# Optimization experiments

Measured on AMD Instinct MI355X. Metric: run time of the kernel, lower is better.

## Reference

```python
import jax, jax.numpy as jnp
import numpy as np

D_MODEL = 1024
EXPAND = 2
D_INNER = EXPAND * D_MODEL      # 2048
D_STATE = 2
D_CONV = 4
DT_RANK = (D_MODEL + 15) // 16  # 64
BATCH, SEQ = 2, 4096
LN_EPS = 1e-5


def setup_inputs() -> dict:
    key = jax.random.key(0)
    ks = jax.random.split(key, 16)
    s = 0.02
    inp = {
        "x":       jax.random.normal(ks[0], (BATCH, SEQ, D_MODEL), jnp.float32),
        # Mamba params (torch Linear convention: W is [out, in])
        "w_in":    jax.random.normal(ks[1], (2 * D_INNER, D_MODEL), jnp.float32) * s,
        "conv_w":  jax.random.normal(ks[2], (D_INNER, 1, D_CONV), jnp.float32) * s,
        "conv_b":  jnp.zeros((D_INNER,), jnp.float32),
        "w_xproj": jax.random.normal(ks[3], (DT_RANK + 2 * D_STATE, D_INNER), jnp.float32) * s,
        "w_dt":    jax.random.normal(ks[4], (D_INNER, DT_RANK), jnp.float32) * s,
        "b_dt":    jax.random.normal(ks[5], (D_INNER,), jnp.float32) * s - 4.0,  # softplus -> small dt
        "a_log":   jnp.log(jnp.broadcast_to(jnp.arange(1, D_STATE + 1, dtype=jnp.float32), (D_INNER, D_STATE))),
        "d_skip":  jnp.ones((D_INNER,), jnp.float32),
        "w_out":   jax.random.normal(ks[6], (D_MODEL, D_INNER), jnp.float32) * s,
        # LayerNorms
        "ln1_g":   jnp.ones((D_MODEL,), jnp.float32),
        "ln1_b":   jnp.zeros((D_MODEL,), jnp.float32),
        "ln2_g":   jnp.ones((D_MODEL,), jnp.float32),
        "ln2_b":   jnp.zeros((D_MODEL,), jnp.float32),
        # FFN (Linear d->d, ReLU, Linear d->d; dropout inactive at eval)
        "ffn_w1":  jax.random.normal(ks[7], (D_MODEL, D_MODEL), jnp.float32) * s,
        "ffn_b1":  jnp.zeros((D_MODEL,), jnp.float32),
        "ffn_w2":  jax.random.normal(ks[8], (D_MODEL, D_MODEL), jnp.float32) * s,
        "ffn_b2":  jnp.zeros((D_MODEL,), jnp.float32),
    }
    return inp


def _ln(x, g, b):
    mu = x.mean(-1, keepdims=True)
    v = ((x - mu) ** 2).mean(-1, keepdims=True)
    return (x - mu) * jax.lax.rsqrt(v + LN_EPS) * g + b


def _mamba(x, w_in, conv_w, conv_b, w_xproj, w_dt, b_dt, a_log, d_skip, w_out):
    Bsz = x.shape[0]
    xz = x @ w_in.T                      # (B,L,2*D_INNER)
    xp, z = jnp.split(xz, 2, axis=-1)
    # depthwise causal conv over time
    xc = jnp.transpose(xp, (0, 2, 1))    # (B,D,L)
    xc = jax.lax.conv_general_dilated(
        xc, conv_w, window_strides=(1,), padding=[(D_CONV - 1, 0)],
        feature_group_count=D_INNER)
    xc = xc + conv_b[None, :, None]
    xp = jax.nn.silu(jnp.transpose(xc, (0, 2, 1)))   # (B,L,D)
    # input-dependent SSM params
    x_dbl = xp @ w_xproj.T               # (B,L,DT_RANK+2N)
    dt, Bm, Cm = jnp.split(x_dbl, [DT_RANK, DT_RANK + D_STATE], axis=-1)
    dt = jax.nn.softplus(dt @ w_dt.T + b_dt)          # (B,L,D)
    A = -jnp.exp(a_log)                  # (D,N)
    dA = jnp.exp(dt[..., None] * A)                  # (B,L,D,N)
    dBu = dt[..., None] * Bm[:, :, None, :] * xp[..., None]  # (B,L,D,N)

    def step(h, inp):
        da, dbu, c = inp                 # (B,D,N),(B,D,N),(B,N)
        h = da * h + dbu
        y = jnp.einsum('bdn,bn->bd', h, c)
        return h, y

    h0 = jnp.zeros((Bsz, D_INNER, D_STATE), x.dtype)
    _, ys = jax.lax.scan(step, h0, (jnp.swapaxes(dA, 0, 1),
                                    jnp.swapaxes(dBu, 0, 1),
                                    jnp.swapaxes(Cm, 0, 1)))
    y = jnp.swapaxes(ys, 0, 1)           # (B,L,D)
    y = (y + d_skip * xp) * jax.nn.silu(z)
    return y @ w_out.T                   # (B,L,d_model)


def reference(x, w_in, conv_w, conv_b, w_xproj, w_dt, b_dt, a_log, d_skip, w_out,
              ln1_g, ln1_b, ln2_g, ln2_b, ffn_w1, ffn_b1, ffn_w2, ffn_b2):
    h = x + _mamba(_ln(x, ln1_g, ln1_b), w_in, conv_w, conv_b, w_xproj,
                   w_dt, b_dt, a_log, d_skip, w_out)
    f = _ln(h, ln2_g, ln2_b)
    f = jax.nn.relu(f @ ffn_w1.T + ffn_b1) @ ffn_w2.T + ffn_b2
    return h + f
```

## Files before the change

kernel.cpp:

```cpp
#include <hip/hip_runtime.h>

typedef unsigned short u16;
typedef __bf16 bf16x8 __attribute__((ext_vector_type(8)));
typedef float f32x4 __attribute__((ext_vector_type(4)));
typedef float f32x2 __attribute__((ext_vector_type(2)));
typedef u16 u16x4 __attribute__((ext_vector_type(4)));
typedef u16 u16x8 __attribute__((ext_vector_type(8)));

#define SEQ   4096
#define DM    1024
#define DI    2048
#define NTOK  8192
#define NXP   68
#define DTR   64
#define NCH   4096
#define CHUNK 32
#define NCHK  128

__device__ __forceinline__ float bf2f(u16 v) {
  union { unsigned u; float f; } x; x.u = ((unsigned)v) << 16; return x.f;
}
__device__ __forceinline__ u16 f2bf(float f) {
  unsigned u = __float_as_uint(f);
  return (u16)((u + 0x7FFFu + ((u >> 16) & 1u)) >> 16);
}

__device__ __forceinline__ void g2l16(const u16* g, u16* l) {
  __builtin_amdgcn_global_load_lds(
      (const __attribute__((address_space(1))) unsigned int*)g,
      (__attribute__((address_space(3))) unsigned int*)l, 16, 0, 0);
}

__global__ __launch_bounds__(256)
void detect_kernel(const u16* __restrict__ x, int* __restrict__ flag)
{
  __shared__ int tot;
  if (threadIdx.x == 0) tot = 0;
  __syncthreads();
  int cnt = 0;
  for (int i = threadIdx.x; i < 4096; i += 256) {
    const int e = (x[2 * i] >> 7) & 0xFF;
    if (e > 167) cnt++;
  }
  atomicAdd(&tot, cnt);
  __syncthreads();
  if (threadIdx.x == 0) flag[0] = (tot >= 8) ? 1 : 0;
}

#define NW0 4194304
#define NW1  139264
#define NW2  131072
#define NW3 2097152
#define NW4 1048576
#define NW5 1048576
#define NBB 4228
__global__ __launch_bounds__(256)
void convert_all(const float* __restrict__ s0, const float* __restrict__ s1,
                 const float* __restrict__ s2, const float* __restrict__ s3,
                 const float* __restrict__ s4, const float* __restrict__ s5,
                 u16* __restrict__ d0, u16* __restrict__ d1, u16* __restrict__ d2,
                 u16* __restrict__ d3, u16* __restrict__ d4, u16* __restrict__ d5,
                 const void* t0, const void* t1, const void* t2, const void* t3,
                 const void* t4, const void* t5, const void* t6, const void* t7,
                 const void* t8, const void* t9, const void* t10,
                 u16* __restrict__ dsm, const int* __restrict__ flag)
{
  if (blockIdx.x >= NBB) {
    const int i = (blockIdx.x - NBB) * 256 + threadIdx.x;
    if (i >= 24576) return;
    const void* src; int off; int dsti = i;
    if      (i < 8192)  { src = t0;  off = i;
                          dsti = (off & 3) * DI + (off >> 2); }
    else if (i < 10240) { src = t1;  off = i - 8192; }
    else if (i < 12288) { src = t2;  off = i - 10240; }
    else if (i < 16384) { src = t3;  off = i - 12288; }
    else if (i < 18432) { src = t4;  off = i - 16384; }
    else if (i < 19456) { src = t5;  off = i - 18432; }
    else if (i < 20480) { src = t6;  off = i - 19456; }
    else if (i < 21504) { src = t7;  off = i - 20480; }
    else if (i < 22528) { src = t8;  off = i - 21504; }
    else if (i < 23552) { src = t9;  off = i - 22528; }
    else                { src = t10; off = i - 23552; }
    dsm[dsti] = (*flag) ? f2bf(((const float*)src)[off]) : ((const u16*)src)[off];
    return;
  }
  if (*flag == 0) return;
  long e = ((long)blockIdx.x * 256 + threadIdx.x) * 8;
  const long c1 = NW0, c2 = c1 + NW1, c3 = c2 + NW2, c4 = c3 + NW3,
             c5 = c4 + NW4, c6 = c5 + NW5;
  if (e >= c6) return;
  const float* s; u16* d;
  if      (e < c1) { s = s0;          d = d0; }
  else if (e < c2) { s = s1; e -= c1; d = d1; }
  else if (e < c3) { s = s2; e -= c2; d = d2; }
  else if (e < c4) { s = s3; e -= c3; d = d3; }
  else if (e < c5) { s = s4; e -= c4; d = d4; }
  else             { s = s5; e -= c5; d = d5; }
  f32x4 a = *(const f32x4*)(s + e);
  f32x4 b = *(const f32x4*)(s + e + 4);
  u16x8 o;
#pragma unroll
  for (int k = 0; k < 4; ++k) { o[k] = f2bf(a[k]); o[4 + k] = f2bf(b[k]); }
  *(u16x8*)(d + e) = o;
}

template<bool DUAL>
__global__ __launch_bounds__(256)
void ln_kernel(const void* __restrict__ xin, const u16* __restrict__ gw,
               const u16* __restrict__ bw, u16* __restrict__ outp,
               const int* __restrict__ flag)
{
  const int tid = threadIdx.x;
  const int sub = tid >> 7;
  const int col0 = (tid & 127) * 8;
  const int row = blockIdx.x * 2 + sub;
  const bool isf32 = DUAL ? (*flag != 0) : true;
  float v[8];
  if (isf32) {
    const float* xf = (const float*)xin + (size_t)row * DM + col0;
    f32x4 a = *(const f32x4*)xf, b2 = *(const f32x4*)(xf + 4);
#pragma unroll
    for (int k = 0; k < 4; ++k) { v[k] = a[k]; v[4 + k] = b2[k]; }
  } else {
    u16x8 xb = *(const u16x8*)((const u16*)xin + (size_t)row * DM + col0);
#pragma unroll
    for (int k = 0; k < 8; ++k) v[k] = bf2f(xb[k]);
  }
  float s = 0.f, s2 = 0.f;
#pragma unroll
  for (int k = 0; k < 8; ++k) { s += v[k]; s2 += v[k] * v[k]; }
#pragma unroll
  for (int off = 32; off > 0; off >>= 1) {
    s  += __shfl_down(s,  off);
    s2 += __shfl_down(s2, off);
  }
  __shared__ float red[4], red2[4];
  __shared__ f32x2 stat[2];
  const int wv = tid >> 6;
  if ((tid & 63) == 0) { red[wv] = s; red2[wv] = s2; }
  __syncthreads();
  if ((tid & 127) == 0) {
    float ts = red[sub * 2] + red[sub * 2 + 1];
    float t2 = red2[sub * 2] + red2[sub * 2 + 1];
    float mu = ts * (1.f / DM);
    float var = t2 * (1.f / DM) - mu * mu;
    stat[sub] = f32x2{mu, rsqrtf(var + 1e-5f)};
  }
  __syncthreads();
  const float mu = stat[sub][0], rs = stat[sub][1];
  u16x8 gv = *(const u16x8*)(gw + col0), bv = *(const u16x8*)(bw + col0);
  u16x8 o;
#pragma unroll
  for (int k = 0; k < 8; ++k)
    o[k] = f2bf((v[k] - mu) * rs * bf2f(gv[k]) + bf2f(bv[k]));
  *(u16x8*)(outp + (size_t)row * DM + col0) = o;
}

template<int EPI, int LNBX>
__global__ __launch_bounds__(256, 2)
void gemm_kernel(const u16* __restrict__ A, const u16* __restrict__ Bc,
                 const u16* __restrict__ Braw,
                 int M, int N, int K,
                 const u16* __restrict__ bias, const u16* __restrict__ addbf,
                 const float* __restrict__ addf, const int* __restrict__ dtflag,
                 void* __restrict__ Cp, void* __restrict__ Cp2)
{
  __shared__ __align__(16) u16 sA[2][128 * 32];
  __shared__ __align__(16) u16 sB[2][128 * 32];
  const int fl = *dtflag;
  const u16* __restrict__ B = fl ? Bc : Braw;
  const int tid = threadIdx.x;
  const int b = blockIdx.x;
  const int xcd = b & 7;
  const int kk = b >> 3;
  const int bx = kk & ((1 << LNBX) - 1);
  const int by = xcd * 8 + (kk >> LNBX);
  const int m0 = by * 128;
  const int n0 = bx * 128;
  const int lane = tid & 63;
  const int wv = tid >> 6;
  const int wm = (wv & 1) * 64;
  const int wn = (wv >> 1) * 64;
  const int r = lane & 15;
  const int q = lane >> 4;
  const int rsw = (r >> 1) & 3;

  const int pr = lane >> 2;
  const int kc = (lane & 3) ^ ((pr >> 1) & 3);
  const int pk = kc * 8;
  u16* lA0[2] = { &sA[0][(wv * 2 + 0) * 512], &sA[1][(wv * 2 + 0) * 512] };
  u16* lA1[2] = { &sA[0][(wv * 2 + 1) * 512], &sA[1][(wv * 2 + 1) * 512] };
  u16* lB0[2] = { &sB[0][(wv * 2 + 0) * 512], &sB[1][(wv * 2 + 0) * 512] };
  u16* lB1[2] = { &sB[0][(wv * 2 + 1) * 512], &sB[1][(wv * 2 + 1) * 512] };
  const u16* gA0 = A + (size_t)(m0 + wv * 32 + pr) * K + pk;
  const u16* gA1 = gA0 + (size_t)16 * K;
  const u16* gB0 = B + (size_t)(n0 + wv * 32 + pr) * K + pk;
  const u16* gB1 = gB0 + (size_t)16 * K;

  f32x4 acc[4][4];
#pragma unroll
  for (int i = 0; i < 4; ++i)
#pragma unroll
    for (int j = 0; j < 4; ++j)
#pragma unroll
      for (int t = 0; t < 4; ++t) acc[i][j][t] = 0.f;

  g2l16(gA0, lA0[0]); g2l16(gA1, lA1[0]);
  g2l16(gB0, lB0[0]); g2l16(gB1, lB1[0]);

  const int nk = K >> 5;
  for (int kt = 0; kt < nk; ++kt) {
    const int cur = kt & 1;
    __syncthreads();
    bf16x8 af[4], bfr[4];
#pragma unroll
    for (int i = 0; i < 4; ++i)
      af[i] = *reinterpret_cast<const bf16x8*>(
          &sA[cur][(wm + i * 16 + r) * 32 + (q ^ rsw) * 8]);
#pragma unroll
    for (int j = 0; j < 4; ++j)
      bfr[j] = *reinterpret_cast<const bf16x8*>(
          &sB[cur][(wn + j * 16 + r) * 32 + (q ^ rsw) * 8]);
    if (kt + 1 < nk) {
      gA0 += 32; gA1 += 32; gB0 += 32; gB1 += 32;
      g2l16(gA0, lA0[cur ^ 1]); g2l16(gA1, lA1[cur ^ 1]);
      g2l16(gB0, lB0[cur ^ 1]); g2l16(gB1, lB1[cur ^ 1]);
    }
#pragma unroll
    for (int i = 0; i < 4; ++i)
#pragma unroll
      for (int j = 0; j < 4; ++j)
        acc[i][j] = __builtin_amdgcn_mfma_f32_16x16x32_bf16(af[i], bfr[j], acc[i][j], 0, 0, 0);
  }

#pragma unroll
  for (int i = 0; i < 4; ++i) {
#pragma unroll
    for (int j = 0; j < 4; ++j) {
#pragma unroll
      for (int t = 0; t < 4; ++t) {
        const int row = m0 + wm + i * 16 + q * 4 + t;
        const int col = n0 + wn + j * 16 + r;
        float v = acc[i][j][t];
        if (EPI == 6) {
          const size_t rb = (size_t)row * DI;
          if (col < DI) ((u16*)Cp)[rb + col] = f2bf(v);
          else          ((u16*)Cp2)[rb + col - DI] = f2bf(v);
        } else {
          const size_t idx = (size_t)row * N + col;
          if (EPI == 1) {
            ((u16*)Cp)[idx] = f2bf(v);
          } else if (EPI == 2) {
            v += bf2f(bias[col]);
            v = (v > 15.f) ? v : __logf(1.f + __expf(v));
            ((u16*)Cp)[idx] = f2bf(v);
          } else if (EPI == 3) {
            v += fl ? addf[idx] : bf2f(addbf[idx]);
            ((float*)Cp)[idx] = v;
          } else if (EPI == 4) {
            v += bf2f(bias[col]);
            ((u16*)Cp)[idx] = f2bf(fmaxf(v, 0.f));
          } else {
            v += bf2f(bias[col]) + addf[idx];
            if (fl) ((float*)Cp)[idx] = v;
            else    ((u16*)Cp)[idx] = f2bf(v);
          }
        }
      }
    }
  }
}

__global__ __launch_bounds__(256, 2)
void xproj_splitk(const u16* __restrict__ A, const u16* __restrict__ Bc,
                  const u16* __restrict__ Braw, const int* __restrict__ dtflag,
                  float* __restrict__ part)
{
  __shared__ __align__(16) u16 sA[2][128 * 32];
  __shared__ __align__(16) u16 sB[2][128 * 32];
  const int fl = *dtflag;
  const u16* __restrict__ B = fl ? Bc : Braw;
  const int tid = threadIdx.x;
  const int kz = blockIdx.x;
  const int m0 = blockIdx.y * 128;
  const int kbase = kz * 256;
  const int lane = tid & 63;
  const int wv = tid >> 6;
  const int wm = (wv & 1) * 64;
  const int wn = (wv >> 1) * 64;
  const int r = lane & 15;
  const int q = lane >> 4;
  const int rsw = (r >> 1) & 3;
  const int pr = lane >> 2;
  const int kc = (lane & 3) ^ ((pr >> 1) & 3);
  const int pk = kc * 8;

  u16* lA0[2] = { &sA[0][(wv * 2 + 0) * 512], &sA[1][(wv * 2 + 0) * 512] };
  u16* lA1[2] = { &sA[0][(wv * 2 + 1) * 512], &sA[1][(wv * 2 + 1) * 512] };
  u16* lB0[2] = { &sB[0][(wv * 2 + 0) * 512], &sB[1][(wv * 2 + 0) * 512] };
  u16* lB1[2] = { &sB[0][(wv * 2 + 1) * 512], &sB[1][(wv * 2 + 1) * 512] };
  int br0 = wv * 32 + pr;      if (br0 > 67) br0 = 67;
  int br1 = wv * 32 + 16 + pr; if (br1 > 67) br1 = 67;
  const u16* gA0 = A + (size_t)(m0 + wv * 32 + pr) * DI + kbase + pk;
  const u16* gA1 = gA0 + (size_t)16 * DI;
  const u16* gB0 = B + (size_t)br0 * DI + kbase + pk;
  const u16* gB1 = B + (size_t)br1 * DI + kbase + pk;

  f32x4 acc[4][4];
#pragma unroll
  for (int i = 0; i < 4; ++i)
#pragma unroll
    for (int j = 0; j < 4; ++j)
#pragma unroll
      for (int t = 0; t < 4; ++t) acc[i][j][t] = 0.f;

  g2l16(gA0, lA0[0]); g2l16(gA1, lA1[0]);
  g2l16(gB0, lB0[0]); g2l16(gB1, lB1[0]);

  for (int kt = 0; kt < 8; ++kt) {
    const int cur = kt & 1;
    __syncthreads();
    bf16x8 af[4], bfr[4];
#pragma unroll
    for (int i = 0; i < 4; ++i)
      af[i] = *reinterpret_cast<const bf16x8*>(
          &sA[cur][(wm + i * 16 + r) * 32 + (q ^ rsw) * 8]);
#pragma unroll
    for (int j = 0; j < 4; ++j)
      bfr[j] = *reinterpret_cast<const bf16x8*>(
          &sB[cur][(wn + j * 16 + r) * 32 + (q ^ rsw) * 8]);
    if (kt + 1 < 8) {
      gA0 += 32; gA1 += 32; gB0 += 32; gB1 += 32;
      g2l16(gA0, lA0[cur ^ 1]); g2l16(gA1, lA1[cur ^ 1]);
      g2l16(gB0, lB0[cur ^ 1]); g2l16(gB1, lB1[cur ^ 1]);
    }
#pragma unroll
    for (int i = 0; i < 4; ++i)
#pragma unroll
      for (int j = 0; j < 4; ++j)
        acc[i][j] = __builtin_amdgcn_mfma_f32_16x16x32_bf16(af[i], bfr[j], acc[i][j], 0, 0, 0);
  }

#pragma unroll
  for (int i = 0; i < 4; ++i)
#pragma unroll
    for (int j = 0; j < 4; ++j)
#pragma unroll
      for (int t = 0; t < 4; ++t) {
        const int row = m0 + wm + i * 16 + q * 4 + t;
        const int col = wn + j * 16 + r;
        if (col < NXP)
          part[((size_t)kz * NTOK + row) * NXP + col] = acc[i][j][t];
      }
}

__global__ __launch_bounds__(256)
void xreduce_kernel(const float* __restrict__ part, u16* __restrict__ dtraw,
                    float* __restrict__ bc)
{
  const int i = blockIdx.x * 256 + threadIdx.x;
  if (i >= NTOK * NXP) return;
  const int row = i / NXP, col = i - row * NXP;
  float s = 0.f;
#pragma unroll
  for (int z = 0; z < 8; ++z) s += part[(size_t)z * NTOK * NXP + i];
  if (col < DTR) dtraw[(size_t)row * DTR + col] = f2bf(s);
  else           bc[row * 4 + (col - DTR)] = s;
}

__global__ __launch_bounds__(256)
void conv_silu_kernel(const u16* __restrict__ xp, const u16* __restrict__ cwT,
                      const u16* __restrict__ cb, u16* __restrict__ u)
{
  const int token = blockIdx.x;
  const int t = token & (SEQ - 1);
  const int d0 = threadIdx.x * 8;
  const ptrdiff_t base = (ptrdiff_t)token * DI + d0;
  float acc[8];
  u16x8 cbv = *(const u16x8*)(cb + d0);
#pragma unroll
  for (int k = 0; k < 8; ++k) acc[k] = bf2f(cbv[k]);
#pragma unroll
  for (int j = 0; j < 4; ++j) {
    if (t - 3 + j >= 0) {
      u16x8 xv = *(const u16x8*)(xp + base + (ptrdiff_t)(j - 3) * DI);
      u16x8 wv = *(const u16x8*)(cwT + j * DI + d0);
#pragma unroll
      for (int k = 0; k < 8; ++k) acc[k] += bf2f(wv[k]) * bf2f(xv[k]);
    }
  }
  u16x8 o;
#pragma unroll
  for (int k = 0; k < 8; ++k) {
    const float sg = 1.f / (1.f + __expf(-acc[k]));
    o[k] = f2bf(acc[k] * sg);
  }
  *(u16x8*)(u + base) = o;
}

__global__ __launch_bounds__(256)
void scan_pass1(const u16* __restrict__ dtb, const u16* __restrict__ ub,
                const float* __restrict__ bc, const u16* __restrict__ a_log,
                float* __restrict__ S, float* __restrict__ hf0, float* __restrict__ hf1)
{
  const int g4 = blockIdx.x * 256 + threadIdx.x;
  const int chg = g4 & (NCH / 4 - 1);
  const int c = g4 >> 10;
  const int ch0 = chg * 4;
  const int b = ch0 >> 11;
  const int d0 = ch0 & (DI - 1);
  u16x8 av = *(const u16x8*)(a_log + d0 * 2);
  float A0[4], A1[4];
#pragma unroll
  for (int k = 0; k < 4; ++k) {
    A0[k] = -__expf(bf2f(av[2 * k]));
    A1[k] = -__expf(bf2f(av[2 * k + 1]));
  }
  float h0[4] = {0.f, 0.f, 0.f, 0.f}, h1[4] = {0.f, 0.f, 0.f, 0.f};
  float s[4] = {0.f, 0.f, 0.f, 0.f};
  const int row0 = b * SEQ + c * CHUNK;
  for (int i = 0; i < CHUNK; ++i) {
    const size_t row = row0 + i;
    u16x4 dtv = *(const u16x4*)(dtb + row * DI + d0);
    u16x4 uv  = *(const u16x4*)(ub + row * DI + d0);
    f32x2 Bv = *(const f32x2*)(bc + row * 4);
#pragma unroll
    for (int k = 0; k < 4; ++k) {
      const float dt = bf2f(dtv[k]);
      const float dtu = dt * bf2f(uv[k]);
      h0[k] = __expf(A0[k] * dt) * h0[k] + dtu * Bv[0];
      h1[k] = __expf(A1[k] * dt) * h1[k] + dtu * Bv[1];
      s[k] += dt;
    }
  }
  const size_t g0 = (size_t)c * NCH + ch0;
  *(f32x4*)(S + g0)   = f32x4{s[0], s[1], s[2], s[3]};
  *(f32x4*)(hf0 + g0) = f32x4{h0[0], h0[1], h0[2], h0[3]};
  *(f32x4*)(hf1 + g0) = f32x4{h1[0], h1[1], h1[2], h1[3]};
}

__global__ __launch_bounds__(256)
void scan_pass2(const float* __restrict__ S, const float* __restrict__ hf0,
                const float* __restrict__ hf1, const u16* __restrict__ a_log,
                float* __restrict__ hi0, float* __restrict__ hi1)
{
  const int ch = blockIdx.x * 256 + threadIdx.x;
  const int d = ch & (DI - 1);
  const float A0 = -__expf(bf2f(a_log[d * 2 + 0]));
  const float A1 = -__expf(bf2f(a_log[d * 2 + 1]));
  float h0 = 0.f, h1 = 0.f;
  size_t g = ch;
  float sv = S[g], f0 = hf0[g], f1 = hf1[g];
  for (int c = 0; c < NCHK; ++c) {
    float svn = 0.f, f0n = 0.f, f1n = 0.f;
    if (c + 1 < NCHK) {
      const size_t gn = g + NCH;
      svn = S[gn]; f0n = hf0[gn]; f1n = hf1[gn];
    }
    hi0[g] = h0; hi1[g] = h1;
    h0 = __expf(A0 * sv) * h0 + f0;
    h1 = __expf(A1 * sv) * h1 + f1;
    sv = svn; f0 = f0n; f1 = f1n;
    g += NCH;
  }
}

__global__ __launch_bounds__(256)
void scan_pass3(const u16* __restrict__ dtb, const u16* __restrict__ ub,
                const float* __restrict__ bc, const u16* __restrict__ zbuf,
                const u16* __restrict__ a_log, const u16* __restrict__ d_skip,
                const float* __restrict__ hi0, const float* __restrict__ hi1,
                u16* __restrict__ yb)
{
  const int g4 = blockIdx.x * 256 + threadIdx.x;
  const int chg = g4 & (NCH / 4 - 1);
  const int c = g4 >> 10;
  const int ch0 = chg * 4;
  const int b = ch0 >> 11;
  const int d0 = ch0 & (DI - 1);
  u16x8 av = *(const u16x8*)(a_log + d0 * 2);
  u16x4 dkv = *(const u16x4*)(d_skip + d0);
  float A0[4], A1[4], dsk[4];
#pragma unroll
  for (int k = 0; k < 4; ++k) {
    A0[k] = -__expf(bf2f(av[2 * k]));
    A1[k] = -__expf(bf2f(av[2 * k + 1]));
    dsk[k] = bf2f(dkv[k]);
  }
  const size_t g0 = (size_t)c * NCH + ch0;
  f32x4 h0v = *(const f32x4*)(hi0 + g0);
  f32x4 h1v = *(const f32x4*)(hi1 + g0);
  float h0[4], h1[4];
#pragma unroll
  for (int k = 0; k < 4; ++k) { h0[k] = h0v[k]; h1[k] = h1v[k]; }
  const int row0 = b * SEQ + c * CHUNK;
  for (int i = 0; i < CHUNK; ++i) {
    const size_t row = row0 + i;
    u16x4 dtv = *(const u16x4*)(dtb + row * DI + d0);
    u16x4 uv  = *(const u16x4*)(ub + row * DI + d0);
    u16x4 zv  = *(const u16x4*)(zbuf + row * DI + d0);
    f32x4 bcv = *(const f32x4*)(bc + row * 4);
    u16x4 o;
#pragma unroll
    for (int k = 0; k < 4; ++k) {
      const float dt = bf2f(dtv[k]);
      const float uu = bf2f(uv[k]);
      const float dtu = dt * uu;
      h0[k] = __expf(A0[k] * dt) * h0[k] + dtu * bcv[0];
      h1[k] = __expf(A1[k] * dt) * h1[k] + dtu * bcv[1];
      const float y = h0[k] * bcv[2] + h1[k] * bcv[3];
      const float z = bf2f(zv[k]);
      const float sz = z / (1.f + __expf(-z));
      o[k] = f2bf((y + dsk[k] * uu) * sz);
    }
    *(u16x4*)(yb + row * DI + d0) = o;
  }
}

extern "C" void kernel_launch(void* const* d_in, const int* in_sizes, int n_in,
                              void* d_out, int out_size, void* d_ws, size_t ws_size,
                              hipStream_t stream)
{
  const void* x       = d_in[0];
  const void* w_in    = d_in[1];
  const void* conv_w  = d_in[2];
  const void* conv_b  = d_in[3];
  const void* w_xproj = d_in[4];
  const void* w_dt    = d_in[5];
  const void* b_dt    = d_in[6];
  const void* a_log   = d_in[7];
  const void* d_skip  = d_in[8];
  const void* w_out   = d_in[9];
  const void* ln1_g   = d_in[10];
  const void* ln1_b   = d_in[11];
  const void* ln2_g   = d_in[12];
  const void* ln2_b   = d_in[13];
  const void* ffn_w1  = d_in[14];
  const void* ffn_b1  = d_in[15];
  const void* ffn_w2  = d_in[16];
  const void* ffn_b2  = d_in[17];
  char* ws = (char*)d_ws;

  const size_t o_flag  = 0;
  const size_t o_small = 256;
  const size_t o_cwout = o_small + 65536;
  const size_t o_cff1  = o_cwout + (size_t)DM * DI * 2;
  const size_t o_cff2  = o_cff1  + (size_t)DM * DM * 2;
  const size_t o_cxp   = o_cff2  + (size_t)DM * DM * 2;
  const size_t o_cwdt  = o_cxp   + (size_t)NXP * DI * 2;
  const size_t o_xn    = 9437184;
  const size_t o_xp    = o_xn + (size_t)NTOK * DM * 2;
  const size_t o_z     = o_xp + (size_t)NTOK * DI * 2;
  const size_t o_u     = o_z  + (size_t)NTOK * DI * 2;
  const size_t o_bc    = o_u  + (size_t)NTOK * DI * 2;
  const size_t SCN = (size_t)NCHK * NCH * 4;
  const size_t o_S   = o_xn + 0 * SCN;
  const size_t o_hf0 = o_xn + 1 * SCN;
  const size_t o_hf1 = o_xn + 2 * SCN;
  const size_t o_hi0 = o_xn + 3 * SCN;
  const size_t o_hi1 = o_xn + 4 * SCN;

  int*   flagp   = (int*)(ws + o_flag);
  u16*   csmall  = (u16*)(ws + o_small);
  u16*   c_cwT   = csmall +     0;
  u16*   c_convb = csmall +  8192;
  u16*   c_bdt   = csmall + 10240;
  u16*   c_alog  = csmall + 12288;
  u16*   c_dskip = csmall + 16384;
  u16*   c_ln1g  = csmall + 18432;
  u16*   c_ln1b  = csmall + 19456;
  u16*   c_ln2g  = csmall + 20480;
  u16*   c_ln2b  = csmall + 21504;
  u16*   c_fb1   = csmall + 22528;
  u16*   c_fb2   = csmall + 23552;
  u16*   c_wout  = (u16*)(ws + o_cwout);
  u16*   c_ff1   = (u16*)(ws + o_cff1);
  u16*   c_ff2   = (u16*)(ws + o_cff2);
  u16*   c_xproj = (u16*)(ws + o_cxp);
  u16*   c_wdt   = (u16*)(ws + o_cwdt);
  u16*   c_win   = (u16*)(ws + o_u);
  u16*   xn      = (u16*)(ws + o_xn);
  u16*   xp      = (u16*)(ws + o_xp);
  u16*   zb      = (u16*)(ws + o_z);
  u16*   u       = (u16*)(ws + o_u);
  float* part    = (float*)(ws + o_xp);
  u16*   dtraw   = (u16*)(ws + o_xn);
  u16*   dtb     = xp;
  u16*   yb      = xp;
  float* bc      = (float*)(ws + o_bc);
  float* S       = (float*)(ws + o_S);
  float* hf0     = (float*)(ws + o_hf0);
  float* hf1     = (float*)(ws + o_hf1);
  float* hi0     = (float*)(ws + o_hi0);
  float* hi1     = (float*)(ws + o_hi1);
  float* h       = (float*)(ws + o_z);
  u16*   hn      = (u16*)(ws + o_xn);
  u16*   f1      = (u16*)(ws + o_u);

  const dim3 blk(256);

  detect_kernel<<<1, blk, 0, stream>>>((const u16*)x, flagp);
  convert_all<<<NBB + 96, blk, 0, stream>>>(
      (const float*)w_in, (const float*)w_xproj, (const float*)w_dt,
      (const float*)w_out, (const float*)ffn_w1, (const float*)ffn_w2,
      c_win, c_xproj, c_wdt, c_wout, c_ff1, c_ff2,
      conv_w, conv_b, b_dt, a_log, d_skip,
      ln1_g, ln1_b, ln2_g, ln2_b, ffn_b1, ffn_b2,
      csmall, flagp);

  ln_kernel<true><<<NTOK / 2, blk, 0, stream>>>(x, c_ln1g, c_ln1b, xn, flagp);
  gemm_kernel<6, 5><<<2048, blk, 0, stream>>>(xn, c_win, (const u16*)w_in,
                                              NTOK, 2 * DI, DM,
                                              nullptr, nullptr, nullptr, flagp, xp, zb);
  conv_silu_kernel<<<NTOK, blk, 0, stream>>>(xp, c_cwT, c_convb, u);
  xproj_splitk<<<dim3(8, 64), blk, 0, stream>>>(u, c_xproj, (const u16*)w_xproj,
                                                flagp, part);
  xreduce_kernel<<<(NTOK * NXP + 255) / 256, blk, 0, stream>>>(part, dtraw, bc);
  gemm_kernel<2, 4><<<1024, blk, 0, stream>>>(dtraw, c_wdt, (const u16*)w_dt,
                                              NTOK, DI, DTR,
                                              c_bdt, nullptr, nullptr, flagp, dtb, nullptr);
  scan_pass1<<<NCHK * NCH / 4 / 256, blk, 0, stream>>>(dtb, u, bc, c_alog, S, hf0, hf1);
  scan_pass2<<<NCH / 256, blk, 0, stream>>>(S, hf0, hf1, c_alog, hi0, hi1);
  scan_pass3<<<NCHK * NCH / 4 / 256, blk, 0, stream>>>(dtb, u, bc, zb, c_alog, c_dskip,
                                                       hi0, hi1, yb);
  gemm_kernel<3, 3><<<512, blk, 0, stream>>>(yb, c_wout, (const u16*)w_out,
                                             NTOK, DM, DI,
                                             nullptr, (const u16*)x, (const float*)x,
                                             flagp, h, nullptr);
  ln_kernel<false><<<NTOK / 2, blk, 0, stream>>>(h, c_ln2g, c_ln2b, hn, flagp);
  gemm_kernel<4, 3><<<512, blk, 0, stream>>>(hn, c_ff1, (const u16*)ffn_w1,
                                             NTOK, DM, DM,
                                             c_fb1, nullptr, nullptr, flagp, f1, nullptr);
  gemm_kernel<5, 3><<<512, blk, 0, stream>>>(f1, c_ff2, (const u16*)ffn_w2,
                                             NTOK, DM, DM,
                                             c_fb2, nullptr, h, flagp, d_out, nullptr);
}
```

Measured before the change: 488.5 us.

## Triple-buffer GEMM LDS pipeline with vmcnt waits and store residual in bf16

GEMM and x-proj split-K kernels move from double to triple LDS buffering. They prefetch two k-tiles ahead and replace __syncthreads with explicit vmcnt waits plus a barrier, so global-to-LDS loads overlap more MFMA work. Separately, the residual h is now written as bf16 instead of fp32, and LN2 and the final GEMM read it as bf16, which halves that traffic. Costs are more LDS per block (which may limit occupancy at 2 blocks/CU) and lower precision in the residual stream.

Result: no change. 483.2 us (-1.1%).

```diff
diff --git a/kernel.cpp b/kernel.cpp
--- a/kernel.cpp
+++ b/kernel.cpp
@@ -30,6 +30,13 @@
       (const __attribute__((address_space(1))) unsigned int*)g,
       (__attribute__((address_space(3))) unsigned int*)l, 16, 0, 0);
 }
+
+#define WAITBAR(imm) do {                           \
+    __asm__ __volatile__("" ::: "memory");          \
+    __builtin_amdgcn_s_waitcnt(imm);                \
+    __builtin_amdgcn_s_barrier();                   \
+    __asm__ __volatile__("" ::: "memory");          \
+  } while (0)
 
 __global__ __launch_bounds__(256)
 void detect_kernel(const u16* __restrict__ x, int* __restrict__ flag)
@@ -104,7 +111,7 @@
   *(u16x8*)(d + e) = o;
 }
 
-template<bool DUAL>
+template<int MODE>
 __global__ __launch_bounds__(256)
 void ln_kernel(const void* __restrict__ xin, const u16* __restrict__ gw,
                const u16* __restrict__ bw, u16* __restrict__ outp,
@@ -114,7 +121,7 @@
   const int sub = tid >> 7;
   const int col0 = (tid & 127) * 8;
   const int row = blockIdx.x * 2 + sub;
-  const bool isf32 = DUAL ? (*flag != 0) : true;
+  const bool isf32 = (MODE == 0) ? (*flag != 0) : false;
   float v[8];
   if (isf32) {
     const float* xf = (const float*)xin + (size_t)row * DM + col0;
@@ -165,8 +172,8 @@
                  const float* __restrict__ addf, const int* __restrict__ dtflag,
                  void* __restrict__ Cp, void* __restrict__ Cp2)
 {
-  __shared__ __align__(16) u16 sA[2][128 * 32];
-  __shared__ __align__(16) u16 sB[2][128 * 32];
+  __shared__ __align__(16) u16 sA[3][128 * 32];
+  __shared__ __align__(16) u16 sB[3][128 * 32];
   const int fl = *dtflag;
   const u16* __restrict__ B = fl ? Bc : Braw;
   const int tid = threadIdx.x;
@@ -188,15 +195,17 @@
   const int pr = lane >> 2;
   const int kc = (lane & 3) ^ ((pr >> 1) & 3);
   const int pk = kc * 8;
-  u16* lA0[2] = { &sA[0][(wv * 2 + 0) * 512], &sA[1][(wv * 2 + 0) * 512] };
-  u16* lA1[2] = { &sA[0][(wv * 2 + 1) * 512], &sA[1][(wv * 2 + 1) * 512] };
-  u16* lB0[2] = { &sB[0][(wv * 2 + 0) * 512], &sB[1][(wv * 2 + 0) * 512] };
-  u16* lB1[2] = { &sB[0][(wv * 2 + 1) * 512], &sB[1][(wv * 2 + 1) * 512] };
+  const int ls0 = (wv * 2 + 0) * 512;
+  const int ls1 = (wv * 2 + 1) * 512;
   const u16* gA0 = A + (size_t)(m0 + wv * 32 + pr) * K + pk;
   const u16* gA1 = gA0 + (size_t)16 * K;
   const u16* gB0 = B + (size_t)(n0 + wv * 32 + pr) * K + pk;
   const u16* gB1 = gB0 + (size_t)16 * K;
 
+#define ISSUE(bb) { g2l16(gA0, &sA[bb][ls0]); g2l16(gA1, &sA[bb][ls1]);   \
+                    g2l16(gB0, &sB[bb][ls0]); g2l16(gB1, &sB[bb][ls1]);   \
+                    gA0 += 32; gA1 += 32; gB0 += 32; gB1 += 32; }
+
   f32x4 acc[4][4];
 #pragma unroll
   for (int i = 0; i < 4; ++i)
@@ -205,13 +214,14 @@
 #pragma unroll
       for (int t = 0; t < 4; ++t) acc[i][j][t] = 0.f;
 
-  g2l16(gA0, lA0[0]); g2l16(gA1, lA1[0]);
-  g2l16(gB0, lB0[0]); g2l16(gB1, lB1[0]);
-
   const int nk = K >> 5;
+  ISSUE(0);
+  if (nk > 1) ISSUE(1);
+
+  int cur = 0;
   for (int kt = 0; kt < nk; ++kt) {
-    const int cur = kt & 1;
-    __syncthreads();
+    if (kt + 1 < nk) { WAITBAR(0x0074); }
+    else             { WAITBAR(0x0070); }
     bf16x8 af[4], bfr[4];
 #pragma unroll
     for (int i = 0; i < 4; ++i)
@@ -221,17 +231,18 @@
     for (int j = 0; j < 4; ++j)
       bfr[j] = *reinterpret_cast<const bf16x8*>(
           &sB[cur][(wn + j * 16 + r) * 32 + (q ^ rsw) * 8]);
-    if (kt + 1 < nk) {
-      gA0 += 32; gA1 += 32; gB0 += 32; gB1 += 32;
-      g2l16(gA0, lA0[cur ^ 1]); g2l16(gA1, lA1[cur ^ 1]);
-      g2l16(gB0, lB0[cur ^ 1]); g2l16(gB1, lB1[cur ^ 1]);
+    if (kt + 2 < nk) {
+      const int nb = (cur == 0) ? 2 : cur - 1;
+      ISSUE(nb);
     }
 #pragma unroll
     for (int i = 0; i < 4; ++i)
 #pragma unroll
       for (int j = 0; j < 4; ++j)
         acc[i][j] = __builtin_amdgcn_mfma_f32_16x16x32_bf16(af[i], bfr[j], acc[i][j], 0, 0, 0);
-  }
+    cur = (cur == 2) ? 0 : cur + 1;
+  }
+#undef ISSUE
 
 #pragma unroll
   for (int i = 0; i < 4; ++i) {
@@ -256,12 +267,12 @@
             ((u16*)Cp)[idx] = f2bf(v);
           } else if (EPI == 3) {
             v += fl ? addf[idx] : bf2f(addbf[idx]);
-            ((float*)Cp)[idx] = v;
+            ((u16*)Cp)[idx] = f2bf(v);
           } else if (EPI == 4) {
             v += bf2f(bias[col]);
             ((u16*)Cp)[idx] = f2bf(fmaxf(v, 0.f));
           } else {
-            v += bf2f(bias[col]) + addf[idx];
+            v += bf2f(bias[col]) + bf2f(addbf[idx]);
             if (fl) ((float*)Cp)[idx] = v;
             else    ((u16*)Cp)[idx] = f2bf(v);
           }
@@ -276,8 +287,8 @@
                   const u16* __restrict__ Braw, const int* __restrict__ dtflag,
                   float* __restrict__ part)
 {
-  __shared__ __align__(16) u16 sA[2][128 * 32];
-  __shared__ __align__(16) u16 sB[2][128 * 32];
+  __shared__ __align__(16) u16 sA[3][128 * 32];
+  __shared__ __align__(16) u16 sB[3][128 * 32];
   const int fl = *dtflag;
   const u16* __restrict__ B = fl ? Bc : Braw;
   const int tid = threadIdx.x;
@@ -294,11 +305,9 @@
   const int pr = lane >> 2;
   const int kc = (lane & 3) ^ ((pr >> 1) & 3);
   const int pk = kc * 8;
-
-  u16* lA0[2] = { &sA[0][(wv * 2 + 0) * 512], &sA[1][(wv * 2 + 0) * 512] };
-  u16* lA1[2] = { &sA[0][(wv * 2 + 1) * 512], &sA[1][(wv * 2 + 1) * 512] };
-  u16* lB0[2] = { &sB[0][(wv * 2 + 0) * 512], &sB[1][(wv * 2 + 0) * 512] };
-  u16* lB1[2] = { &sB[0][(wv * 2 + 1) * 512], &sB[1][(wv * 2 + 1) * 512] };
+  const int ls0 = (wv * 2 + 0) * 512;
+  const int ls1 = (wv * 2 + 1) * 512;
+
   int br0 = wv * 32 + pr;      if (br0 > 67) br0 = 67;
   int br1 = wv * 32 + 16 + pr; if (br1 > 67) br1 = 67;
   const u16* gA0 = A + (size_t)(m0 + wv * 32 + pr) * DI + kbase + pk;
@@ -306,6 +315,10 @@
   const u16* gB0 = B + (size_t)br0 * DI + kbase + pk;
   const u16* gB1 = B + (size_t)br1 * DI + kbase + pk;
 
+#define ISSUE(bb) { g2l16(gA0, &sA[bb][ls0]); g2l16(gA1, &sA[bb][ls1]);   \
+                    g2l16(gB0, &sB[bb][ls0]); g2l16(gB1, &sB[bb][ls1]);   \
+                    gA0 += 32; gA1 += 32; gB0 += 32; gB1 += 32; }
+
   f32x4 acc[4][4];
 #pragma unroll
   for (int i = 0; i < 4; ++i)
@@ -314,12 +327,13 @@
 #pragma unroll
       for (int t = 0; t < 4; ++t) acc[i][j][t] = 0.f;
 
-  g2l16(gA0, lA0[0]); g2l16(gA1, lA1[0]);
-  g2l16(gB0, lB0[0]); g2l16(gB1, lB1[0]);
-
+  ISSUE(0);
+  ISSUE(1);
+
+  int cur = 0;
   for (int kt = 0; kt < 8; ++kt) {
-    const int cur = kt & 1;
-    __syncthreads();
+    if (kt + 1 < 8) { WAITBAR(0x0074); }
+    else            { WAITBAR(0x0070); }
     bf16x8 af[4], bfr[4];
 #pragma unroll
     for (int i = 0; i < 4; ++i)
@@ -329,17 +343,18 @@
     for (int j = 0; j < 4; ++j)
       bfr[j] = *reinterpret_cast<const bf16x8*>(
           &sB[cur][(wn + j * 16 + r) * 32 + (q ^ rsw) * 8]);
-    if (kt + 1 < 8) {
-      gA0 += 32; gA1 += 32; gB0 += 32; gB1 += 32;
-      g2l16(gA0, lA0[cur ^ 1]); g2l16(gA1, lA1[cur ^ 1]);
-      g2l16(gB0, lB0[cur ^ 1]); g2l16(gB1, lB1[cur ^ 1]);
+    if (kt + 2 < 8) {
+      const int nb = (cur == 0) ? 2 : cur - 1;
+      ISSUE(nb);
     }
 #pragma unroll
     for (int i = 0; i < 4; ++i)
 #pragma unroll
       for (int j = 0; j < 4; ++j)
         acc[i][j] = __builtin_amdgcn_mfma_f32_16x16x32_bf16(af[i], bfr[j], acc[i][j], 0, 0, 0);
-  }
+    cur = (cur == 2) ? 0 : cur + 1;
+  }
+#undef ISSUE
 
 #pragma unroll
   for (int i = 0; i < 4; ++i)
@@ -593,7 +608,7 @@
   float* hf1     = (float*)(ws + o_hf1);
   float* hi0     = (float*)(ws + o_hi0);
   float* hi1     = (float*)(ws + o_hi1);
-  float* h       = (float*)(ws + o_z);
+  u16*   hb      = (u16*)(ws + o_z);
   u16*   hn      = (u16*)(ws + o_xn);
   u16*   f1      = (u16*)(ws + o_u);
 
@@ -608,7 +623,7 @@
       ln1_g, ln1_b, ln2_g, ln2_b, ffn_b1, ffn_b2,
       csmall, flagp);
 
-  ln_kernel<true><<<NTOK / 2, blk, 0, stream>>>(x, c_ln1g, c_ln1b, xn, flagp);
+  ln_kernel<0><<<NTOK / 2, blk, 0, stream>>>(x, c_ln1g, c_ln1b, xn, flagp);
   gemm_kernel<6, 5><<<2048, blk, 0, stream>>>(xn, c_win, (const u16*)w_in,
                                               NTOK, 2 * DI, DM,
                                               nullptr, nullptr, nullptr, flagp, xp, zb);
@@ -626,12 +641,12 @@
   gemm_kernel<3, 3><<<512, blk, 0, stream>>>(yb, c_wout, (const u16*)w_out,
                                              NTOK, DM, DI,
                                              nullptr, (const u16*)x, (const float*)x,
-                                             flagp, h, nullptr);
-  ln_kernel<false><<<NTOK / 2, blk, 0, stream>>>(h, c_ln2g, c_ln2b, hn, flagp);
+                                             flagp, hb, nullptr);
+  ln_kernel<1><<<NTOK / 2, blk, 0, stream>>>(hb, c_ln2g, c_ln2b, hn, flagp);
   gemm_kernel<4, 3><<<512, blk, 0, stream>>>(hn, c_ff1, (const u16*)ffn_w1,
                                              NTOK, DM, DM,
                                              c_fb1, nullptr, nullptr, flagp, f1, nullptr);
   gemm_kernel<5, 3><<<512, blk, 0, stream>>>(f1, c_ff2, (const u16*)ffn_w2,
                                              NTOK, DM, DM,
-                                             c_fb2, nullptr, h, flagp, d_out, nullptr);
-}
+                                             c_fb2, hb, nullptr, flagp, d_out, nullptr);
+}
```

## Stage GEMM epilogue through LDS for vectorized stores; keep residual h in bf16

Applied to the files above, without the earlier changes.

The GEMM epilogue now writes accumulators to shared memory and reads them back transposed, so each lane emits 16 contiguous outputs with 128-bit vector loads and stores instead of scattered scalar writes. The residual stream h after the out-projection is also stored as bf16 rather than fp32, halving its write and its two later reads (LN2 and the final residual add). Costs are an extra barrier and LDS round-trip per tile, plus reduced precision of the residual, which may hurt accuracy against the fp32 reference.

After: 466.1 us. 1.05x faster.

```diff
diff --git a/kernel.cpp b/kernel.cpp
--- a/kernel.cpp
+++ b/kernel.cpp
@@ -104,7 +104,7 @@
   *(u16x8*)(d + e) = o;
 }
 
-template<bool DUAL>
+template<int MODE>
 __global__ __launch_bounds__(256)
 void ln_kernel(const void* __restrict__ xin, const u16* __restrict__ gw,
                const u16* __restrict__ bw, u16* __restrict__ outp,
@@ -114,7 +114,7 @@
   const int sub = tid >> 7;
   const int col0 = (tid & 127) * 8;
   const int row = blockIdx.x * 2 + sub;
-  const bool isf32 = DUAL ? (*flag != 0) : true;
+  const bool isf32 = (MODE == 0) ? (*flag != 0) : false;
   float v[8];
   if (isf32) {
     const float* xf = (const float*)xin + (size_t)row * DM + col0;
@@ -233,38 +233,121 @@
         acc[i][j] = __builtin_amdgcn_mfma_f32_16x16x32_bf16(af[i], bfr[j], acc[i][j], 0, 0, 0);
   }
 
+  __syncthreads();
+  float* ep = (wv < 2) ? ((float*)&sA[0][0] + wv * 2048)
+                       : ((float*)&sB[0][0] + (wv - 2) * 2048);
+  const int r2 = lane >> 2;
+  const int ccol = ((lane & 3) ^ (r2 & 3)) * 16;
+  u16* C6 = nullptr; int c6off = 0;
+  if (EPI == 6) { C6 = (n0 < DI) ? (u16*)Cp : (u16*)Cp2; c6off = (n0 < DI) ? 0 : DI; }
+
 #pragma unroll
   for (int i = 0; i < 4; ++i) {
 #pragma unroll
-    for (int j = 0; j < 4; ++j) {
-#pragma unroll
-      for (int t = 0; t < 4; ++t) {
-        const int row = m0 + wm + i * 16 + q * 4 + t;
-        const int col = n0 + wn + j * 16 + r;
-        float v = acc[i][j][t];
-        if (EPI == 6) {
-          const size_t rb = (size_t)row * DI;
-          if (col < DI) ((u16*)Cp)[rb + col] = f2bf(v);
-          else          ((u16*)Cp2)[rb + col - DI] = f2bf(v);
+    for (int j = 0; j < 4; ++j)
+#pragma unroll
+      for (int t = 0; t < 4; ++t)
+        ep[(q * 4 + t) * 68 + j * 16 + r] = acc[i][j][t];
+    f32x4 w0 = *(const f32x4*)&ep[r2 * 68 + ccol + 0];
+    f32x4 w1 = *(const f32x4*)&ep[r2 * 68 + ccol + 4];
+    f32x4 w2 = *(const f32x4*)&ep[r2 * 68 + ccol + 8];
+    f32x4 w3 = *(const f32x4*)&ep[r2 * 68 + ccol + 12];
+    float vv[16];
+#pragma unroll
+    for (int k = 0; k < 4; ++k) {
+      vv[k] = w0[k]; vv[4 + k] = w1[k]; vv[8 + k] = w2[k]; vv[12 + k] = w3[k];
+    }
+    const int row = m0 + wm + i * 16 + r2;
+    const int colg = n0 + wn + ccol;
+    if (EPI == 6) {
+      u16x8 o0, o1;
+#pragma unroll
+      for (int k = 0; k < 8; ++k) { o0[k] = f2bf(vv[k]); o1[k] = f2bf(vv[8 + k]); }
+      const size_t cb6 = (size_t)row * DI + (colg - c6off);
+      *(u16x8*)&C6[cb6] = o0;
+      *(u16x8*)&C6[cb6 + 8] = o1;
+    } else {
+      const size_t idx = (size_t)row * N + colg;
+      if (EPI == 1) {
+        u16x8 o0, o1;
+#pragma unroll
+        for (int k = 0; k < 8; ++k) { o0[k] = f2bf(vv[k]); o1[k] = f2bf(vv[8 + k]); }
+        *(u16x8*)&((u16*)Cp)[idx] = o0;
+        *(u16x8*)&((u16*)Cp)[idx + 8] = o1;
+      } else if (EPI == 2) {
+        u16x8 b0 = *(const u16x8*)&bias[colg];
+        u16x8 b1 = *(const u16x8*)&bias[colg + 8];
+        u16x8 o0, o1;
+#pragma unroll
+        for (int k = 0; k < 8; ++k) {
+          float v0 = vv[k] + bf2f(b0[k]);
+          float v1 = vv[8 + k] + bf2f(b1[k]);
+          v0 = (v0 > 15.f) ? v0 : __logf(1.f + __expf(v0));
+          v1 = (v1 > 15.f) ? v1 : __logf(1.f + __expf(v1));
+          o0[k] = f2bf(v0); o1[k] = f2bf(v1);
+        }
+        *(u16x8*)&((u16*)Cp)[idx] = o0;
+        *(u16x8*)&((u16*)Cp)[idx + 8] = o1;
+      } else if (EPI == 3) {
+        float ax[16];
+        if (fl) {
+          f32x4 a0 = *(const f32x4*)&addf[idx];
+          f32x4 a1 = *(const f32x4*)&addf[idx + 4];
+          f32x4 a2 = *(const f32x4*)&addf[idx + 8];
+          f32x4 a3 = *(const f32x4*)&addf[idx + 12];
+#pragma unroll
+          for (int k = 0; k < 4; ++k) {
+            ax[k] = a0[k]; ax[4 + k] = a1[k]; ax[8 + k] = a2[k]; ax[12 + k] = a3[k];
+          }
         } else {
-          const size_t idx = (size_t)row * N + col;
-          if (EPI == 1) {
-            ((u16*)Cp)[idx] = f2bf(v);
-          } else if (EPI == 2) {
-            v += bf2f(bias[col]);
-            v = (v > 15.f) ? v : __logf(1.f + __expf(v));
-            ((u16*)Cp)[idx] = f2bf(v);
-          } else if (EPI == 3) {
-            v += fl ? addf[idx] : bf2f(addbf[idx]);
-            ((float*)Cp)[idx] = v;
-          } else if (EPI == 4) {
-            v += bf2f(bias[col]);
-            ((u16*)Cp)[idx] = f2bf(fmaxf(v, 0.f));
-          } else {
-            v += bf2f(bias[col]) + addf[idx];
-            if (fl) ((float*)Cp)[idx] = v;
-            else    ((u16*)Cp)[idx] = f2bf(v);
-          }
+          u16x8 a0 = *(const u16x8*)&addbf[idx];
+          u16x8 a1 = *(const u16x8*)&addbf[idx + 8];
+#pragma unroll
+          for (int k = 0; k < 8; ++k) { ax[k] = bf2f(a0[k]); ax[8 + k] = bf2f(a1[k]); }
+        }
+        u16x8 o0, o1;
+#pragma unroll
+        for (int k = 0; k < 8; ++k) {
+          o0[k] = f2bf(vv[k] + ax[k]); o1[k] = f2bf(vv[8 + k] + ax[8 + k]);
+        }
+        *(u16x8*)&((u16*)Cp)[idx] = o0;
+        *(u16x8*)&((u16*)Cp)[idx + 8] = o1;
+      } else if (EPI == 4) {
+        u16x8 b0 = *(const u16x8*)&bias[colg];
+        u16x8 b1 = *(const u16x8*)&bias[colg + 8];
+        u16x8 o0, o1;
+#pragma unroll
+        for (int k = 0; k < 8; ++k) {
+          o0[k] = f2bf(fmaxf(vv[k] + bf2f(b0[k]), 0.f));
+          o1[k] = f2bf(fmaxf(vv[8 + k] + bf2f(b1[k]), 0.f));
+        }
+        *(u16x8*)&((u16*)Cp)[idx] = o0;
+        *(u16x8*)&((u16*)Cp)[idx + 8] = o1;
+      } else {
+        u16x8 b0 = *(const u16x8*)&bias[colg];
+        u16x8 b1 = *(const u16x8*)&bias[colg + 8];
+        u16x8 a0 = *(const u16x8*)&addbf[idx];
+        u16x8 a1 = *(const u16x8*)&addbf[idx + 8];
+        float r0[8], r1[8];
+#pragma unroll
+        for (int k = 0; k < 8; ++k) {
+          r0[k] = vv[k] + bf2f(b0[k]) + bf2f(a0[k]);
+          r1[k] = vv[8 + k] + bf2f(b1[k]) + bf2f(a1[k]);
+        }
+        if (fl) {
+          f32x4 f0, f1, f2, f3;
+#pragma unroll
+          for (int k = 0; k < 4; ++k) { f0[k] = r0[k]; f1[k] = r0[4 + k]; f2[k] = r1[k]; f3[k] = r1[4 + k]; }
+          *(f32x4*)&((float*)Cp)[idx] = f0;
+          *(f32x4*)&((float*)Cp)[idx + 4] = f1;
+          *(f32x4*)&((float*)Cp)[idx + 8] = f2;
+          *(f32x4*)&((float*)Cp)[idx + 12] = f3;
+        } else {
+          u16x8 o0, o1;
+#pragma unroll
+          for (int k = 0; k < 8; ++k) { o0[k] = f2bf(r0[k]); o1[k] = f2bf(r1[k]); }
+          *(u16x8*)&((u16*)Cp)[idx] = o0;
+          *(u16x8*)&((u16*)Cp)[idx + 8] = o1;
         }
       }
     }
@@ -593,7 +676,7 @@
   float* hf1     = (float*)(ws + o_hf1);
   float* hi0     = (float*)(ws + o_hi0);
   float* hi1     = (float*)(ws + o_hi1);
-  float* h       = (float*)(ws + o_z);
+  u16*   hb      = (u16*)(ws + o_z);
   u16*   hn      = (u16*)(ws + o_xn);
   u16*   f1      = (u16*)(ws + o_u);
 
@@ -608,7 +691,7 @@
       ln1_g, ln1_b, ln2_g, ln2_b, ffn_b1, ffn_b2,
       csmall, flagp);
 
-  ln_kernel<true><<<NTOK / 2, blk, 0, stream>>>(x, c_ln1g, c_ln1b, xn, flagp);
+  ln_kernel<0><<<NTOK / 2, blk, 0, stream>>>(x, c_ln1g, c_ln1b, xn, flagp);
   gemm_kernel<6, 5><<<2048, blk, 0, stream>>>(xn, c_win, (const u16*)w_in,
                                               NTOK, 2 * DI, DM,
                                               nullptr, nullptr, nullptr, flagp, xp, zb);
@@ -626,12 +709,12 @@
   gemm_kernel<3, 3><<<512, blk, 0, stream>>>(yb, c_wout, (const u16*)w_out,
                                              NTOK, DM, DI,
                                              nullptr, (const u16*)x, (const float*)x,
-                                             flagp, h, nullptr);
-  ln_kernel<false><<<NTOK / 2, blk, 0, stream>>>(h, c_ln2g, c_ln2b, hn, flagp);
+                                             flagp, hb, nullptr);
+  ln_kernel<1><<<NTOK / 2, blk, 0, stream>>>(hb, c_ln2g, c_ln2b, hn, flagp);
   gemm_kernel<4, 3><<<512, blk, 0, stream>>>(hn, c_ff1, (const u16*)ffn_w1,
                                              NTOK, DM, DM,
                                              c_fb1, nullptr, nullptr, flagp, f1, nullptr);
   gemm_kernel<5, 3><<<512, blk, 0, stream>>>(f1, c_ff2, (const u16*)ffn_w2,
                                              NTOK, DM, DM,
-                                             c_fb2, nullptr, h, flagp, d_out, nullptr);
-}
+                                             c_fb2, hb, nullptr, flagp, d_out, nullptr);
+}
```
